# Kernel tuning notes

Hardware: AMD Instinct MI355X
Metric: run time of the kernel (lower is better)

Reference implementation:

```python
import jax, jax.numpy as jnp
import numpy as np

N, C, T, V, D = 64, 64, 256, 25, 64
BN_EPS = 1e-5


def _make_shift(v, ch, sign):
    idx = np.empty(v * ch, dtype=np.int64)
    for i in range(v):
        for j in range(ch):
            idx[i * ch + j] = (i * ch + j + sign * j * ch) % (ch * v)
    return jnp.asarray(idx, dtype=jnp.int32)


def setup_inputs() -> dict:
    key = jax.random.key(0)
    ks = jax.random.split(key, 8)
    return {
        "x0": jax.random.normal(ks[0], (N, C, T, V), dtype=jnp.float32),
        "fc1_w": jax.random.normal(ks[1], (C // 4, C), dtype=jnp.float32) * (1.0 / np.sqrt(C)),
        "fc1_b": jnp.zeros((C // 4,), dtype=jnp.float32),
        "fc2_w": jax.random.normal(ks[2], (4, C // 4), dtype=jnp.float32) * (1.0 / np.sqrt(C // 4)),
        "fc2_b": jnp.zeros((4,), dtype=jnp.float32),
        "Linear_weight": jax.random.normal(ks[3], (4, C, D), dtype=jnp.float32) * np.sqrt(1.0 / D),
        "Linear_bias": jax.random.normal(ks[4], (4, D), dtype=jnp.float32) * 0.02,
        "Feature_Mask": jax.random.normal(ks[5], (1, V, C), dtype=jnp.float32) * 0.1,
        "bn_gamma": 1.0 + 0.05 * jax.random.normal(ks[6], (V * D,), dtype=jnp.float32),
        "bn_beta": 0.05 * jax.random.normal(ks[7], (V * D,), dtype=jnp.float32),
        "shift_in": _make_shift(V, C, +1),
        "shift_out": _make_shift(V, D, -1),
        "epoch": 100,
    }


def reference(x0, fc1_w, fc1_b, fc2_w, fc2_b, Linear_weight, Linear_bias,
              Feature_Mask, bn_gamma, bn_beta, shift_in, shift_out, epoch):
    n, c, t, v = x0.shape
    d = Linear_weight.shape[-1]

    # DY_SEModule gate: global avg pool -> 1x1 convs -> tempered softmax over 4
    pooled = x0.mean(axis=(2, 3))                       # [n, c]
    h = jax.nn.relu(pooled @ fc1_w.T + fc1_b)           # [n, c//4]
    logits = h @ fc2_w.T + fc2_b                        # [n, 4]
    tao = (-(30.0 - 1.0) / 60.0 * epoch + 30.0) if epoch < 60 else 1.0
    gate = jax.nn.softmax(logits / tao, axis=1)         # [n, 4]

    # per-sample fused weights / bias
    W_fuse = jnp.einsum('kcd,nk->ncd', Linear_weight, gate)   # [n, c, d]
    b_fuse = jnp.einsum('kc,nk->nc', Linear_bias, gate)       # [n, d]

    # shift-in gather over flattened (v*c) channel axis
    x = x0.transpose(0, 2, 3, 1).reshape(n * t, v * c)  # [n*t, v*c]
    x = x[:, shift_in].reshape(n * t, v, c)
    x = x * (jnp.tanh(Feature_Mask) + 1.0)              # learnable feature mask
    x = x.reshape(n, t, v, c)

    # per-sample dynamic linear + bias
    x = jnp.einsum('ntvc,ncd->ntvd', x, W_fuse) + b_fuse[:, None, None, :]

    # shift-out gather
    x = x.reshape(n * t, v * d)[:, shift_out]           # [n*t, v*d]

    # BatchNorm1d (training mode: batch statistics over n*t)
    mean = x.mean(axis=0)
    var = jnp.var(x, axis=0)
    x = (x - mean) * jax.lax.rsqrt(var + BN_EPS) * bn_gamma + bn_beta

    x = x.reshape(n, t, v, d).transpose(0, 3, 1, 2)     # [n, d, t, v]
    return jax.nn.relu(x + x0)                          # identity residual (c == d)
```

## Files before the change

### kernel.cpp

```cpp
#include <hip/hip_runtime.h>
#include <hip/hip_bf16.h>
#include <math.h>

#define NN 64
#define CC 64
#define TT 256
#define VV 25
#define DD 64
#define BN_EPS 1e-5f
#define NREP 16

typedef short bf16x8 __attribute__((ext_vector_type(8)));
typedef float f32x4 __attribute__((ext_vector_type(4)));

#define WS_POOLED 0
#define WS_GATE   4096
#define WS_BFUSE  4352
#define WS_MASK   8448
#define WS_ABP    10048
#define WS_S1     13248
#define WS_S2     38848
#define WS_WTB    64448
#define WS_YB     195520

static __device__ __forceinline__ unsigned short f2bf(float x) {
    __hip_bfloat16 h = __float2bfloat16(x);
    return *(unsigned short*)&h;
}
static __device__ __forceinline__ float bf2f(unsigned short u) {
    return __uint_as_float(((unsigned)u) << 16);
}
static __device__ __forceinline__ void gload_lds16(const void* gsrc, void* ldst) {
    typedef const __attribute__((address_space(1))) unsigned int gu32;
    typedef __attribute__((address_space(3))) unsigned int lu32;
    __builtin_amdgcn_global_load_lds((gu32*)gsrc, (lu32*)ldst, 16, 0, 0);
}

__global__ __launch_bounds__(256) void k_mask(const float* __restrict__ fmask, float* ws) {
    const int f = blockIdx.x * 256 + threadIdx.x;
    if (f < VV * CC) ws[WS_MASK + f] = tanhf(fmask[f]) + 1.0f;
}

__global__ __launch_bounds__(256) void k_xt(const float* __restrict__ x0,
                                            const float* __restrict__ ws,
                                            float* __restrict__ pooled,
                                            unsigned short* __restrict__ xT) {
    __shared__ __align__(16) float tile[64][104];
    const int n = blockIdx.y, tcb = blockIdx.x;
    const int tid = threadIdx.x;
    const size_t nbase = (size_t)n * (CC * TT * VV);
    const int col0 = tcb * 100;

    for (int l4 = tid; l4 < 1600; l4 += 256) {
        const int c = l4 / 25, q = l4 - c * 25;
        const float4 v = *(const float4*)(x0 + nbase + c * 6400 + col0 + 4 * q);
        *(float4*)&tile[c][4 * q] = v;
    }
    __syncthreads();

    if (tid < 64) {
        float s = 0.f;
        for (int q = 0; q < 25; q++) {
            const float4 v = *(const float4*)&tile[tid][4 * q];
            s += v.x + v.y + v.z + v.w;
        }
        atomicAdd(&pooled[n * 64 + tid], s * (1.f / 6400.f));
    }

    const float* maskg = ws + WS_MASK;
    for (int l = tid; l < 800; l += 256) {
        const int row = l >> 3;
        const int jb = (l & 7) * 8;
        const int trel = row / 25, i = row - trel * 25;
        const float4 m0 = *(const float4*)(maskg + i * 64 + jb);
        const float4 m1 = *(const float4*)(maskg + i * 64 + jb + 4);
        const float mk[8] = {m0.x, m0.y, m0.z, m0.w, m1.x, m1.y, m1.z, m1.w};
        unsigned outw[4];
#pragma unroll
        for (int pair = 0; pair < 4; pair++) {
            unsigned lo = 0, hi = 0;
#pragma unroll
            for (int hl = 0; hl < 2; hl++) {
                const int j = jb + pair * 2 + hl;
                int jm = j; if (jm >= 50) jm -= 50; else if (jm >= 25) jm -= 25;
                int p = i + jm; if (p >= 25) p -= 25;
                const float v = tile[j][trel * 25 + p] * mk[pair * 2 + hl];
                if (hl == 0) lo = (unsigned)f2bf(v); else hi = (unsigned)f2bf(v);
            }
            outw[pair] = lo | (hi << 16);
        }
        const int grow = col0 + row;
        const int jswz = ((l & 7) ^ (grow & 7)) * 8;
        *(uint4*)(xT + ((size_t)(n * 6400) + grow) * 64 + jswz) = *(uint4*)outw;
    }
}

__global__ __launch_bounds__(256) void k_gate(const float* __restrict__ fc1_w,
                                              const float* __restrict__ fc1_b,
                                              const float* __restrict__ fc2_w,
                                              const float* __restrict__ fc2_b,
                                              const float* __restrict__ lin_b,
                                              const int* __restrict__ epoch_p,
                                              float* ws) {
    const int tid = threadIdx.x;
    float* pooled = ws + WS_POOLED;
    float* gate   = ws + WS_GATE;
    float* bfuse  = ws + WS_BFUSE;

    if (tid < 64) {
        const int n = tid;
        const float* po = pooled + n * 64;
        float h[16];
        for (int q = 0; q < 16; q++) {
            float z = fc1_b[q];
            for (int j = 0; j < 64; j++) z = fmaf(fc1_w[q * 64 + j], po[j], z);
            h[q] = fmaxf(z, 0.f);
        }
        float lg[4];
        for (int k = 0; k < 4; k++) {
            float z = fc2_b[k];
            for (int q = 0; q < 16; q++) z = fmaf(fc2_w[k * 16 + q], h[q], z);
            lg[k] = z;
        }
        const int ep = epoch_p[0];
        const float tao = (ep < 60) ? (-(29.0f / 60.0f) * (float)ep + 30.0f) : 1.0f;
        float mx = -1e30f;
        for (int k = 0; k < 4; k++) { lg[k] /= tao; mx = fmaxf(mx, lg[k]); }
        float se = 0.f;
        for (int k = 0; k < 4; k++) { lg[k] = expf(lg[k] - mx); se += lg[k]; }
        const float inv = 1.f / se;
        for (int k = 0; k < 4; k++) gate[n * 4 + k] = lg[k] * inv;
    }
    __syncthreads();
    for (int f = tid; f < 4096; f += 256) {
        const int n = f >> 6, d = f & 63;
        float s = 0.f;
        for (int k = 0; k < 4; k++) s = fmaf(lin_b[k * 64 + d], gate[n * 4 + k], s);
        bfuse[f] = s;
    }
}

__global__ __launch_bounds__(256) void k_wfuse(const float* __restrict__ lw, float* ws) {
    __shared__ float tile[64 * 65];
    const float* gate = ws + WS_GATE;
    unsigned short* wtb = (unsigned short*)(ws + WS_WTB);
    const int n = blockIdx.x;
    float g[4];
    for (int k = 0; k < 4; k++) g[k] = gate[n * 4 + k];
    for (int f = threadIdx.x; f < 4096; f += 256) {
        const int c = f >> 6, d = f & 63;
        float v = g[0] * lw[f] + g[1] * lw[4096 + f] + g[2] * lw[8192 + f] + g[3] * lw[12288 + f];
        tile[d * 65 + c] = v;
    }
    __syncthreads();
    for (int f = threadIdx.x; f < 4096; f += 256) {
        const int d = f >> 6, c = f & 63;
        wtb[n * 4096 + f] = f2bf(tile[d * 65 + c]);
    }
}

__global__ __launch_bounds__(256) void k_gemm(const unsigned short* __restrict__ xT,
                                              const unsigned short* __restrict__ wtb,
                                              const float* __restrict__ ws,
                                              float* __restrict__ wsmut) {
    __shared__ __align__(16) char pool[45568];
    const int n = blockIdx.y, tb = blockIdx.x;
    const int tid = threadIdx.x;
    const int wv = tid >> 6, lane = tid & 63;
    const int lrow = lane & 15, lgrp = lane >> 4;
    const int dcol = wv * 16 + lrow;

    unsigned short* outw = (unsigned short*)(pool + 32768) + wv * 1600;

    const bf16x8 w0 = *(const bf16x8*)(wtb + n * 4096 + dcol * 64 + 8 * lgrp);
    const bf16x8 w1 = *(const bf16x8*)(wtb + n * 4096 + dcol * 64 + 32 + 8 * lgrp);
    const float bfv = ws[WS_BFUSE + n * 64 + dcol];
    asm volatile("" ::: "memory");

    const char* xbase = (const char*)(xT + (size_t)n * 6400 * 64);
    {
        const char* src = xbase + (size_t)(tb * 400) * 128;
#pragma unroll
        for (int it = 0; it < 4; it++)
            gload_lds16(src + it * 4096 + tid * 16, pool + it * 4096 + tid * 16);
    }
    asm volatile("" ::: "memory");
    {
        const char* src = xbase + (size_t)(tb * 400 + 100) * 128;
#pragma unroll
        for (int it = 0; it < 4; it++)
            gload_lds16(src + it * 4096 + tid * 16, pool + 16384 + it * 4096 + tid * 16);
    }
    asm volatile("s_waitcnt vmcnt(4)" ::: "memory");
    asm volatile("s_barrier" ::: "memory");

    float s1r[7][4], s2r[7][4];
#pragma unroll
    for (int m = 0; m < 7; m++)
#pragma unroll
        for (int r = 0; r < 4; r++) { s1r[m][r] = 0.f; s2r[m][r] = 0.f; }

    unsigned short* yg = (unsigned short*)(wsmut + WS_YB) + (size_t)n * 64 * 6400;

#pragma unroll
    for (int ck = 0; ck < 4; ck++) {
        const int rowt = tb * 400 + ck * 100;
        const unsigned short* Xm = (const unsigned short*)(pool + (ck & 1) * 16384);
        const int b7 = (ck & 1) * 4;

#pragma unroll
        for (int m = 0; m < 7; m++) {
            const int rloc = m * 16 + lrow;
            const int r7 = (rloc + b7) & 7;
            const bf16x8 a0 = *(const bf16x8*)(Xm + rloc * 64 + ((lgrp ^ r7) << 3));
            const bf16x8 a1 = *(const bf16x8*)(Xm + rloc * 64 + (((lgrp + 4) ^ r7) << 3));
            f32x4 a = {bfv, bfv, bfv, bfv};
            a = __builtin_amdgcn_mfma_f32_16x16x32_bf16(a0, w0, a, 0, 0, 0);
            a = __builtin_amdgcn_mfma_f32_16x16x32_bf16(a1, w1, a, 0, 0, 0);
#pragma unroll
            for (int r = 0; r < 4; r++) {
                const int row = m * 16 + 4 * lgrp + r;
                if (row < 100) {
                    const unsigned short us = f2bf(a[r]);
                    const float yf = bf2f(us);
                    s1r[m][r] += yf;
                    s2r[m][r] = fmaf(yf, yf, s2r[m][r]);
                    outw[lrow * 100 + row] = us;
                }
            }
        }
#pragma unroll
        for (int it = 0; it < 7; it++) {
            const int l = lane + it * 64;
            if (l < 400) {
                const int dloc = l / 25, q = l - dloc * 25;
                const uint2 u = *(const uint2*)(outw + dloc * 100 + 4 * q);
                *(uint2*)(yg + (size_t)(wv * 16 + dloc) * 6400 + rowt + 4 * q) = u;
            }
        }
        if (ck < 3) {
            asm volatile("s_waitcnt vmcnt(7)" ::: "memory");
            asm volatile("s_barrier" ::: "memory");
            if (ck < 2) {
                const char* src = xbase + (size_t)(tb * 400 + (ck + 2) * 100) * 128;
                char* dst = pool + (ck & 1) * 16384;
#pragma unroll
                for (int it = 0; it < 4; it++)
                    gload_lds16(src + it * 4096 + tid * 16, dst + it * 4096 + tid * 16);
            }
        }
    }

    __syncthreads();
    float* s1l = (float*)pool;
    float* s2l = s1l + 1650;
    for (int f = tid; f < 3300; f += 256) s1l[f] = 0.f;
    __syncthreads();
#pragma unroll
    for (int m = 0; m < 7; m++) {
#pragma unroll
        for (int r = 0; r < 4; r++) {
            const int row = m * 16 + 4 * lgrp + r;
            if (row < 100) {
                int vv = row;
                if (vv >= 75) vv -= 75; else if (vv >= 50) vv -= 50; else if (vv >= 25) vv -= 25;
                __hip_atomic_fetch_add(&s1l[vv * 66 + dcol], s1r[m][r],
                                       __ATOMIC_RELAXED, __HIP_MEMORY_SCOPE_WORKGROUP);
                __hip_atomic_fetch_add(&s2l[vv * 66 + dcol], s2r[m][r],
                                       __ATOMIC_RELAXED, __HIP_MEMORY_SCOPE_WORKGROUP);
            }
        }
    }
    __syncthreads();
    const int rep = (n * 5 + tb) & (NREP - 1);
    float* g1 = wsmut + WS_S1 + rep * 1600;
    float* g2 = wsmut + WS_S2 + rep * 1600;
    for (int f = tid; f < 1600; f += 256) {
        atomicAdd(&g1[f], s1l[(f >> 6) * 66 + (f & 63)]);
        atomicAdd(&g2[f], s2l[(f >> 6) * 66 + (f & 63)]);
    }
}

__global__ __launch_bounds__(256) void k_finalize(const float* __restrict__ gamma,
                                                  const float* __restrict__ beta,
                                                  float* ws) {
    const int f = blockIdx.x * 256 + threadIdx.x;
    if (f >= VV * DD) return;
    const int v = f >> 6, d = f & 63;
    const int vi = (v - d + 175) % 25;
    const int fin = vi * 64 + d;
    float s1 = 0.f, s2 = 0.f;
    for (int rep = 0; rep < NREP; rep++) {
        s1 += ws[WS_S1 + rep * 1600 + fin];
        s2 += ws[WS_S2 + rep * 1600 + fin];
    }
    const float mean = s1 * (1.f / (NN * TT));
    float var = s2 * (1.f / (NN * TT)) - mean * mean;
    var = fmaxf(var, 0.f);
    const float rs = rsqrtf(var + BN_EPS);
    const float a = gamma[f] * rs;
    const float b = beta[f] - mean * a;
    ((unsigned*)ws)[WS_ABP + f] = (unsigned)f2bf(a) | (((unsigned)f2bf(b)) << 16);
}

__global__ __launch_bounds__(256) void k_bn(const float* __restrict__ x0,
                                            const float* __restrict__ ws,
                                            float* __restrict__ out) {
    __shared__ __align__(16) unsigned short ybL[6400];
    __shared__ float aL[25], bL[25];
    const int d = blockIdx.x, n = blockIdx.y;
    const int tid = threadIdx.x;
    const size_t pbase = (size_t)(n * 64 + d) * 6400;
    const unsigned short* yb = (const unsigned short*)(ws + WS_YB);

    for (int l = tid; l < 800; l += 256)
        *(uint4*)&ybL[l * 8] = *(const uint4*)(yb + pbase + l * 8);
    if (tid < 25) {
        const unsigned u = ((const unsigned*)ws)[WS_ABP + tid * 64 + d];
        aL[tid] = __uint_as_float(u << 16);
        bL[tid] = __uint_as_float(u & 0xffff0000u);
    }
    __syncthreads();

    const int sh = d % 25;
    for (int l4 = tid; l4 < 1600; l4 += 256) {
        const int e0 = 4 * l4;
        const float4 xv = *(const float4*)(x0 + pbase + e0);
        int t = e0 / 25;
        int vo = e0 - 25 * t;
        float o[4];
        const float xe[4] = {xv.x, xv.y, xv.z, xv.w};
#pragma unroll
        for (int k = 0; k < 4; k++) {
            int vs = vo - sh; if (vs < 0) vs += 25;
            const float y = bf2f(ybL[t * 25 + vs]);
            o[k] = fmaxf(fmaf(aL[vo], y, bL[vo]) + xe[k], 0.f);
            vo++; if (vo >= 25) { vo = 0; t++; }
        }
        float4 ov = {o[0], o[1], o[2], o[3]};
        *(float4*)(out + pbase + e0) = ov;
    }
}

extern "C" void kernel_launch(void* const* d_in, const int* in_sizes, int n_in,
                              void* d_out, int out_size, void* d_ws, size_t ws_size,
                              hipStream_t stream) {
    const float* x0    = (const float*)d_in[0];
    const float* fc1_w = (const float*)d_in[1];
    const float* fc1_b = (const float*)d_in[2];
    const float* fc2_w = (const float*)d_in[3];
    const float* fc2_b = (const float*)d_in[4];
    const float* lw    = (const float*)d_in[5];
    const float* lb    = (const float*)d_in[6];
    const float* fmask = (const float*)d_in[7];
    const float* gamma = (const float*)d_in[8];
    const float* beta  = (const float*)d_in[9];
    const int* epoch   = (const int*)d_in[12];
    float* ws  = (float*)d_ws;
    float* out = (float*)d_out;
    unsigned short* xT = (unsigned short*)d_out;
    const unsigned short* wtb = (const unsigned short*)(ws + WS_WTB);

    hipMemsetAsync(d_ws, 0, (size_t)WS_WTB * sizeof(float), stream);

    k_mask<<<7, 256, 0, stream>>>(fmask, ws);
    k_xt<<<dim3(64, 64), 256, 0, stream>>>(x0, ws, ws + WS_POOLED, xT);
    k_gate<<<1, 256, 0, stream>>>(fc1_w, fc1_b, fc2_w, fc2_b, lb, epoch, ws);
    k_wfuse<<<NN, 256, 0, stream>>>(lw, ws);
    k_gemm<<<dim3(16, 64), 256, 0, stream>>>(xT, wtb, ws, ws);
    k_finalize<<<7, 256, 0, stream>>>(gamma, beta, ws);
    k_bn<<<dim3(64, 64), 256, 0, stream>>>(x0, ws, out);
}
```

Baseline: 211.5 us.

## Split GEMM into smaller 128-row tiles with more blocks and stat replicas

The GEMM kernel now gives each block a single 128-row tile (grid 50x64) instead of 400 rows in four double-buffered chunks (grid 16x64). This drops the in-kernel load pipelining and the row<100 guards, and uses a smaller LDS footprint. The aim is higher occupancy and more parallel blocks. The BN-statistics replicas double to 32 to spread the global atomic contention from the extra blocks. In exchange, every block pays the full load latency up front and performs more shared and global atomics in total.

```diff
diff --git a/kernel.cpp b/kernel.cpp
--- a/kernel.cpp
+++ b/kernel.cpp
@@ -8,7 +8,7 @@
 #define VV 25
 #define DD 64
 #define BN_EPS 1e-5f
-#define NREP 16
+#define NREP 32
 
 typedef short bf16x8 __attribute__((ext_vector_type(8)));
 typedef float f32x4 __attribute__((ext_vector_type(4)));
@@ -19,9 +19,9 @@
 #define WS_MASK   8448
 #define WS_ABP    10048
 #define WS_S1     13248
-#define WS_S2     38848
-#define WS_WTB    64448
-#define WS_YB     195520
+#define WS_S2     64448
+#define WS_WTB    115648
+#define WS_YB     246720
 
 static __device__ __forceinline__ unsigned short f2bf(float x) {
     __hip_bfloat16 h = __float2bfloat16(x);
@@ -163,92 +163,61 @@
                                               const unsigned short* __restrict__ wtb,
                                               const float* __restrict__ ws,
                                               float* __restrict__ wsmut) {
-    __shared__ __align__(16) char pool[45568];
+    __shared__ __align__(16) char pool[33792];
+    unsigned short* Xm = (unsigned short*)pool;
     const int n = blockIdx.y, tb = blockIdx.x;
+    const int rowbase = tb * 128;
     const int tid = threadIdx.x;
     const int wv = tid >> 6, lane = tid & 63;
     const int lrow = lane & 15, lgrp = lane >> 4;
     const int dcol = wv * 16 + lrow;
 
-    unsigned short* outw = (unsigned short*)(pool + 32768) + wv * 1600;
+    unsigned short* outw = (unsigned short*)(pool + 16384) + wv * 2176;
 
     const bf16x8 w0 = *(const bf16x8*)(wtb + n * 4096 + dcol * 64 + 8 * lgrp);
     const bf16x8 w1 = *(const bf16x8*)(wtb + n * 4096 + dcol * 64 + 32 + 8 * lgrp);
     const float bfv = ws[WS_BFUSE + n * 64 + dcol];
-    asm volatile("" ::: "memory");
-
-    const char* xbase = (const char*)(xT + (size_t)n * 6400 * 64);
+
     {
-        const char* src = xbase + (size_t)(tb * 400) * 128;
+        const char* src = (const char*)(xT + ((size_t)n * 6400 + rowbase) * 64);
 #pragma unroll
         for (int it = 0; it < 4; it++)
             gload_lds16(src + it * 4096 + tid * 16, pool + it * 4096 + tid * 16);
     }
-    asm volatile("" ::: "memory");
-    {
-        const char* src = xbase + (size_t)(tb * 400 + 100) * 128;
-#pragma unroll
-        for (int it = 0; it < 4; it++)
-            gload_lds16(src + it * 4096 + tid * 16, pool + 16384 + it * 4096 + tid * 16);
-    }
-    asm volatile("s_waitcnt vmcnt(4)" ::: "memory");
-    asm volatile("s_barrier" ::: "memory");
-
-    float s1r[7][4], s2r[7][4];
-#pragma unroll
-    for (int m = 0; m < 7; m++)
+    __syncthreads();
+
+    float s1r[8][4], s2r[8][4];
+#pragma unroll
+    for (int m = 0; m < 8; m++)
 #pragma unroll
         for (int r = 0; r < 4; r++) { s1r[m][r] = 0.f; s2r[m][r] = 0.f; }
 
-    unsigned short* yg = (unsigned short*)(wsmut + WS_YB) + (size_t)n * 64 * 6400;
-
-#pragma unroll
-    for (int ck = 0; ck < 4; ck++) {
-        const int rowt = tb * 400 + ck * 100;
-        const unsigned short* Xm = (const unsigned short*)(pool + (ck & 1) * 16384);
-        const int b7 = (ck & 1) * 4;
-
-#pragma unroll
-        for (int m = 0; m < 7; m++) {
-            const int rloc = m * 16 + lrow;
-            const int r7 = (rloc + b7) & 7;
-            const bf16x8 a0 = *(const bf16x8*)(Xm + rloc * 64 + ((lgrp ^ r7) << 3));
-            const bf16x8 a1 = *(const bf16x8*)(Xm + rloc * 64 + (((lgrp + 4) ^ r7) << 3));
-            f32x4 a = {bfv, bfv, bfv, bfv};
-            a = __builtin_amdgcn_mfma_f32_16x16x32_bf16(a0, w0, a, 0, 0, 0);
-            a = __builtin_amdgcn_mfma_f32_16x16x32_bf16(a1, w1, a, 0, 0, 0);
-#pragma unroll
-            for (int r = 0; r < 4; r++) {
-                const int row = m * 16 + 4 * lgrp + r;
-                if (row < 100) {
-                    const unsigned short us = f2bf(a[r]);
-                    const float yf = bf2f(us);
-                    s1r[m][r] += yf;
-                    s2r[m][r] = fmaf(yf, yf, s2r[m][r]);
-                    outw[lrow * 100 + row] = us;
-                }
-            }
-        }
-#pragma unroll
-        for (int it = 0; it < 7; it++) {
-            const int l = lane + it * 64;
-            if (l < 400) {
-                const int dloc = l / 25, q = l - dloc * 25;
-                const uint2 u = *(const uint2*)(outw + dloc * 100 + 4 * q);
-                *(uint2*)(yg + (size_t)(wv * 16 + dloc) * 6400 + rowt + 4 * q) = u;
-            }
-        }
-        if (ck < 3) {
-            asm volatile("s_waitcnt vmcnt(7)" ::: "memory");
-            asm volatile("s_barrier" ::: "memory");
-            if (ck < 2) {
-                const char* src = xbase + (size_t)(tb * 400 + (ck + 2) * 100) * 128;
-                char* dst = pool + (ck & 1) * 16384;
-#pragma unroll
-                for (int it = 0; it < 4; it++)
-                    gload_lds16(src + it * 4096 + tid * 16, dst + it * 4096 + tid * 16);
-            }
-        }
+    const int r7 = lrow & 7;
+#pragma unroll
+    for (int m = 0; m < 8; m++) {
+        const int rloc = m * 16 + lrow;
+        const bf16x8 a0 = *(const bf16x8*)(Xm + rloc * 64 + ((lgrp ^ r7) << 3));
+        const bf16x8 a1 = *(const bf16x8*)(Xm + rloc * 64 + (((lgrp + 4) ^ r7) << 3));
+        f32x4 a = {bfv, bfv, bfv, bfv};
+        a = __builtin_amdgcn_mfma_f32_16x16x32_bf16(a0, w0, a, 0, 0, 0);
+        a = __builtin_amdgcn_mfma_f32_16x16x32_bf16(a1, w1, a, 0, 0, 0);
+#pragma unroll
+        for (int r = 0; r < 4; r++) {
+            const int row = m * 16 + 4 * lgrp + r;
+            const unsigned short us = f2bf(a[r]);
+            const float yf = bf2f(us);
+            s1r[m][r] += yf;
+            s2r[m][r] = fmaf(yf, yf, s2r[m][r]);
+            outw[lrow * 136 + row] = us;
+        }
+    }
+    unsigned short* yg = (unsigned short*)(wsmut + WS_YB) + (size_t)n * 64 * 6400 + rowbase;
+#pragma unroll
+    for (int it = 0; it < 8; it++) {
+        const int l = lane + it * 64;
+        const int dloc = l >> 5, q = l & 31;
+        const uint2 u = *(const uint2*)(outw + dloc * 136 + 4 * q);
+        *(uint2*)(yg + (size_t)(wv * 16 + dloc) * 6400 + 4 * q) = u;
     }
 
     __syncthreads();
@@ -256,23 +225,23 @@
     float* s2l = s1l + 1650;
     for (int f = tid; f < 3300; f += 256) s1l[f] = 0.f;
     __syncthreads();
-#pragma unroll
-    for (int m = 0; m < 7; m++) {
+    const int vbase = rowbase % 25;
+#pragma unroll
+    for (int m = 0; m < 8; m++) {
 #pragma unroll
         for (int r = 0; r < 4; r++) {
             const int row = m * 16 + 4 * lgrp + r;
-            if (row < 100) {
-                int vv = row;
-                if (vv >= 75) vv -= 75; else if (vv >= 50) vv -= 50; else if (vv >= 25) vv -= 25;
-                __hip_atomic_fetch_add(&s1l[vv * 66 + dcol], s1r[m][r],
-                                       __ATOMIC_RELAXED, __HIP_MEMORY_SCOPE_WORKGROUP);
-                __hip_atomic_fetch_add(&s2l[vv * 66 + dcol], s2r[m][r],
-                                       __ATOMIC_RELAXED, __HIP_MEMORY_SCOPE_WORKGROUP);
-            }
-        }
-    }
-    __syncthreads();
-    const int rep = (n * 5 + tb) & (NREP - 1);
+            int vv = vbase + row;
+            vv -= (vv >= 125) ? 125 : (vv >= 100) ? 100 : (vv >= 75) ? 75 :
+                  (vv >= 50) ? 50 : (vv >= 25) ? 25 : 0;
+            __hip_atomic_fetch_add(&s1l[vv * 66 + dcol], s1r[m][r],
+                                   __ATOMIC_RELAXED, __HIP_MEMORY_SCOPE_WORKGROUP);
+            __hip_atomic_fetch_add(&s2l[vv * 66 + dcol], s2r[m][r],
+                                   __ATOMIC_RELAXED, __HIP_MEMORY_SCOPE_WORKGROUP);
+        }
+    }
+    __syncthreads();
+    const int rep = (n * 50 + tb) & (NREP - 1);
     float* g1 = wsmut + WS_S1 + rep * 1600;
     float* g2 = wsmut + WS_S2 + rep * 1600;
     for (int f = tid; f < 1600; f += 256) {
@@ -367,7 +336,7 @@
     k_xt<<<dim3(64, 64), 256, 0, stream>>>(x0, ws, ws + WS_POOLED, xT);
     k_gate<<<1, 256, 0, stream>>>(fc1_w, fc1_b, fc2_w, fc2_b, lb, epoch, ws);
     k_wfuse<<<NN, 256, 0, stream>>>(lw, ws);
-    k_gemm<<<dim3(16, 64), 256, 0, stream>>>(xT, wtb, ws, ws);
+    k_gemm<<<dim3(50, 64), 256, 0, stream>>>(xT, wtb, ws, ws);
     k_finalize<<<7, 256, 0, stream>>>(gamma, beta, ws);
     k_bn<<<dim3(64, 64), 256, 0, stream>>>(x0, ws, out);
 }
```

New measurement: 410.3 us. 94.0% more time.
